# Performance work log

Measured on AMD Instinct MI355X. Metric: run time of the kernel, lower is better.

Reference implementation:

```python
import jax, jax.numpy as jnp
import numpy as np

FEATURE_DIM = 128
VALUE_DIM = 128


def setup_inputs() -> dict:
    key = jax.random.key(0)
    k1, k2, k3 = jax.random.split(key, 3)
    BH, S = 32, 4096
    q = jax.random.normal(k1, (BH, S, FEATURE_DIM), dtype=jnp.float32)
    k = jax.random.normal(k2, (BH, S, FEATURE_DIM), dtype=jnp.float32)
    v = jax.random.normal(k3, (BH, S, VALUE_DIM), dtype=jnp.float32)
    return {"q": q, "k": k, "v": v, "chunk_size": 128}


def reference(q, k, v, chunk_size):
    # q,k: [BH,S,F]; v: [BH,S,V]. Chunked fast-weight linear-attention scan:
    # out_t = q_t . (sum_{s<=t} k_s (x) v_s) / t
    BH, S, F = q.shape
    V = v.shape[-1]
    C = max(1, int(chunk_size))
    assert S % C == 0, "seq_len must be divisible by chunk_size for this reference"
    n_chunks = S // C
    # [n_chunks, BH, C, dim] for lax.scan over chunks
    qc = q.reshape(BH, n_chunks, C, F).transpose(1, 0, 2, 3)
    kc = k.reshape(BH, n_chunks, C, F).transpose(1, 0, 2, 3)
    vc = v.reshape(BH, n_chunks, C, V).transpose(1, 0, 2, 3)

    w0 = jnp.zeros((BH, F, V), dtype=q.dtype)

    def step(w_state, inputs):
        qi, ki, vi = inputs  # [BH,C,F], [BH,C,F], [BH,C,V]
        kv = jnp.einsum('bnf,bnv->bnfv', ki, vi)          # [BH,C,F,V]
        w_prefix = jnp.cumsum(kv, axis=1) + w_state[:, None]  # inclusive prefix sums
        out = jnp.einsum('bnf,bnfv->bnv', qi, w_prefix)    # [BH,C,V]
        return w_prefix[:, -1], out

    _, outs = jax.lax.scan(step, w0, (qc, kc, vc))
    out = outs.transpose(1, 0, 2, 3).reshape(BH, S, V)
    inv_counts = 1.0 / jnp.arange(1, S + 1, dtype=q.dtype)
    return out * inv_counts[None, :, None]
```

## Files before the change

### kernel.cpp

```cpp
#include <hip/hip_runtime.h>


typedef _Float16 f16;
typedef __attribute__((ext_vector_type(2))) _Float16 f16x2;
typedef __attribute__((ext_vector_type(4))) _Float16 f16x4;
typedef __attribute__((ext_vector_type(8))) _Float16 f16x8;
typedef __attribute__((ext_vector_type(16))) float f32x16;
typedef __attribute__((ext_vector_type(4))) float fv4;
typedef __attribute__((ext_vector_type(4))) int i32x4;

#define MFMA32(a, b, c) __builtin_amdgcn_mfma_f32_32x32x16_f16((a), (b), (c), 0, 0, 0)

__device__ __forceinline__ f16x4 cvt4(fv4 x) {
  f16x2 lo = __builtin_bit_cast(f16x2, __builtin_amdgcn_cvt_pkrtz(x[0], x[1]));
  f16x2 hi = __builtin_bit_cast(f16x2, __builtin_amdgcn_cvt_pkrtz(x[2], x[3]));
  return __builtin_shufflevector(lo, hi, 0, 1, 2, 3);
}

__device__ __forceinline__ int swzb(int row, int col) {
  int s = (row ^ (row >> 3)) & 7;
  return (row << 8) + ((col << 1) ^ (s << 4));
}

__device__ __forceinline__ f16x8 frag32(const f16* lds, int row, int kk, int lane) {
  int c0 = (kk << 4) + ((lane >> 5) << 3);
  return *(const f16x8*)((const char*)lds + swzb(row, c0));
}

__device__ __forceinline__ int rowf(int r, int g) {
  return (r & 3) + ((r >> 2) << 3) + (g << 2);
}

__global__ __launch_bounds__(512, 1)
void ttr_pt(const float* __restrict__ k, const float* __restrict__ v,
            f16* __restrict__ pt) {
  __shared__ f16 kT[128 * 128];
  __shared__ f16 vT[128 * 128];
  const int tid = threadIdx.x, lane = tid & 63, wave = tid >> 6;
  const int bh = blockIdx.x >> 5, c = blockIdx.x & 31;
  const float* kg = k + ((size_t)bh * 4096 + c * 128) * 128;
  const float* vg = v + ((size_t)bh * 4096 + c * 128) * 128;
  const int f0 = (tid & 31) << 2;
#pragma unroll
  for (int p = 0; p < 8; ++p) {
    int s = (p << 4) + (tid >> 5);
    fv4 xk = *(const fv4*)(kg + s * 128 + f0);
    fv4 xv = *(const fv4*)(vg + s * 128 + f0);
#pragma unroll
    for (int e = 0; e < 4; ++e) {
      *(f16*)((char*)kT + swzb(f0 + e, s)) = (f16)xk[e];
      *(f16*)((char*)vT + swzb(f0 + e, s)) = (f16)xv[e];
    }
  }
  __syncthreads();
  const int l31 = lane & 31, g = lane >> 5;
  const int mt = wave >> 1, nt0 = (wave & 1) << 1;
  f32x16 p0 = {0.f}, p1 = {0.f};
#pragma unroll
  for (int kk = 0; kk < 8; ++kk) {
    f16x8 a = frag32(vT, (mt << 5) + l31, kk, lane);
    p0 = MFMA32(a, frag32(kT, (nt0 << 5) + l31, kk, lane), p0);
    p1 = MFMA32(a, frag32(kT, ((nt0 + 1) << 5) + l31, kk, lane), p1);
  }
  f16* dst = pt + (size_t)blockIdx.x * 16384;
#pragma unroll
  for (int r = 0; r < 16; ++r) {
    int vr = (mt << 5) + rowf(r, g);
    dst[vr * 128 + (nt0 << 5) + l31] = (f16)p0[r];
    dst[vr * 128 + ((nt0 + 1) << 5) + l31] = (f16)p1[r];
  }
}

__global__ __launch_bounds__(256, 1)
void ttr_prefix(const f16* __restrict__ pt, f16* __restrict__ w) {
  __shared__ f16 xch[256 * 8];
  const int tid = threadIdx.x;
  const int bh = blockIdx.x >> 3, vs = blockIdx.x & 7;
  const int v0 = vs << 4;
  const int NT = v0 >> 5;
  const int vloc = tid >> 4, fblk = tid & 15;
  const size_t bhbase = (size_t)bh * 32 * 16384;
  const f16* src = pt + bhbase + (size_t)(v0 + vloc) * 128 + fblk * 8;
  const int kk = tid >> 5, gg = (tid >> 4) & 1, lc = tid & 15;
  f16* dstu = w + bhbase +
              (size_t)(((NT * 8 + kk) * 64) + gg * 32 + (v0 & 31) + lc) * 8;
  const int phi_w = vloc * 16 + (fblk ^ vloc);
  const int phi_r = lc * 16 + ((tid >> 4) ^ lc);
  float acc[8];
#pragma unroll
  for (int e = 0; e < 8; ++e) acc[e] = 0.f;
  for (int c = 0; c < 32; ++c) {
    f16x8 pcur = *(const f16x8*)(src + (size_t)c * 16384);
    f16x8 h;
#pragma unroll
    for (int e = 0; e < 8; ++e) h[e] = (f16)acc[e];
    *(f16x8*)(xch + phi_w * 8) = h;
    __syncthreads();
    f16x8 o = *(const f16x8*)(xch + phi_r * 8);
    *(f16x8*)(dstu + (size_t)c * 16384) = o;
    __syncthreads();
#pragma unroll
    for (int e = 0; e < 8; ++e) acc[e] += (float)pcur[e];
  }
}

__global__ __launch_bounds__(256, 3)
void ttr_out(const float* __restrict__ q, const float* __restrict__ k,
             const float* __restrict__ v, const f16* __restrict__ w,
             float* __restrict__ out) {
  __shared__ f16 k_lds[128 * 128];
  __shared__ f16 vT[64 * 128];
  const int tid = threadIdx.x, lane = tid & 63, wave = tid >> 6;
  const int l31 = lane & 31, g = lane >> 5;
  const int widx = blockIdx.x & 15;
  const int gidx = ((blockIdx.x >> 4) << 3) + (widx & 7);
  const int vh = widx >> 3;
  const int bh = gidx >> 5, c = gidx & 31;
  const float* qg = q + ((size_t)bh * 4096 + c * 128) * 128;
  const float* kg = k + ((size_t)bh * 4096 + c * 128) * 128;
  const float* vg = v + ((size_t)bh * 4096 + c * 128) * 128 + vh * 64;

  const f16* wsrc = w + (size_t)gidx * 16384 + (size_t)(vh * 2) * 4096;
  f16x8 wf0[8], wf1[8];
#pragma unroll
  for (int kk = 0; kk < 8; ++kk) {
    wf0[kk] = *(const f16x8*)(wsrc + (size_t)((kk << 6) + lane) * 8);
    wf1[kk] = *(const f16x8*)(wsrc + (size_t)(4096 + ((kk << 6) + lane) * 8));
  }

  f16x8 qf[8];
  {
    const float* qr = qg + ((wave << 5) + l31) * 128 + (g << 3);
#pragma unroll
    for (int kk = 0; kk < 8; ++kk) {
      f16x4 a = cvt4(*(const fv4*)(qr + (kk << 4)));
      f16x4 b = cvt4(*(const fv4*)(qr + (kk << 4) + 4));
      qf[kk] = __builtin_shufflevector(a, b, 0, 1, 2, 3, 4, 5, 6, 7);
    }
  }
  {
    const int c0 = (tid & 31) << 2;
#pragma unroll
    for (int p = 0; p < 16; ++p) {
      int s = (p << 3) + (tid >> 5);
      *(f16x4*)((char*)k_lds + swzb(s, c0)) = cvt4(*(const fv4*)(kg + s * 128 + c0));
    }
  }
  {
    const int c0 = (tid & 15) << 2;
#pragma unroll
    for (int p = 0; p < 8; ++p) {
      int s = (p << 4) + (tid >> 4);
      fv4 xv = *(const fv4*)(vg + s * 128 + c0);
#pragma unroll
      for (int e = 0; e < 4; ++e)
        *(f16*)((char*)vT + swzb(c0 + e, s)) = (f16)xv[e];
    }
  }
  __syncthreads();

  f32x16 o0 = {0.f}, o1 = {0.f};
#pragma unroll
  for (int kk = 0; kk < 8; ++kk) {
    o0 = MFMA32(qf[kk], wf0[kk], o0);
    o1 = MFMA32(qf[kk], wf1[kk], o1);
  }

  for (int j = 0; j <= wave; ++j) {
    f32x16 sa = {0.f};
#pragma unroll
    for (int kk = 0; kk < 8; ++kk)
      sa = MFMA32(frag32(k_lds, (j << 5) + l31, kk, lane), qf[kk], sa);
    if (j == wave) {
#pragma unroll
      for (int r = 0; r < 16; ++r)
        if (rowf(r, g) > l31) sa[r] = 0.f;
    }
    int wds[8];
#pragma unroll
    for (int t = 0; t < 8; ++t)
      wds[t] = __builtin_bit_cast(
          int, __builtin_amdgcn_cvt_pkrtz(sa[2 * t], sa[2 * t + 1]));
    int rA = __shfl_xor(g ? wds[0] : wds[2], 32, 64);
    int rB = __shfl_xor(g ? wds[1] : wds[3], 32, 64);
    int rC = __shfl_xor(g ? wds[4] : wds[6], 32, 64);
    int rD = __shfl_xor(g ? wds[5] : wds[7], 32, 64);
    i32x4 P0 = {g ? rA : wds[0], g ? rB : wds[1],
                g ? wds[2] : rA, g ? wds[3] : rB};
    i32x4 P1 = {g ? rC : wds[4], g ? rD : wds[5],
                g ? wds[6] : rC, g ? wds[7] : rD};
    f16x8 pa0 = __builtin_bit_cast(f16x8, P0);
    f16x8 pa1 = __builtin_bit_cast(f16x8, P1);
    o0 = MFMA32(pa0, frag32(vT, l31, (j << 1), lane), o0);
    o0 = MFMA32(pa1, frag32(vT, l31, (j << 1) + 1, lane), o0);
    o1 = MFMA32(pa0, frag32(vT, 32 + l31, (j << 1), lane), o1);
    o1 = MFMA32(pa1, frag32(vT, 32 + l31, (j << 1) + 1, lane), o1);
  }

  float* og = out + (((size_t)bh * 4096) + c * 128 + (wave << 5)) * 128 + vh * 64;
#pragma unroll
  for (int r = 0; r < 16; ++r) {
    int rl = rowf(r, g);
    float tg = (float)(c * 128 + (wave << 5) + rl + 1);
    float rcp = __builtin_amdgcn_rcpf(tg);
    og[rl * 128 + l31] = o0[r] * rcp;
    og[rl * 128 + 32 + l31] = o1[r] * rcp;
  }
}

extern "C" void kernel_launch(void* const* d_in, const int* in_sizes, int n_in,
                              void* d_out, int out_size, void* d_ws, size_t ws_size,
                              hipStream_t stream) {
  const float* q = (const float*)d_in[0];
  const float* k = (const float*)d_in[1];
  const float* v = (const float*)d_in[2];
  float* o = (float*)d_out;
  f16* pt = (f16*)d_ws;
  f16* w = pt + (size_t)32 * 32 * 16384;
  ttr_pt<<<dim3(1024), dim3(512), 0, stream>>>(k, v, pt);
  ttr_prefix<<<dim3(256), dim3(256), 0, stream>>>(pt, w);
  ttr_out<<<dim3(2048), dim3(256), 0, stream>>>(q, k, v, w, o);
}
```

Measured before the change: 96.07 us.

## Stage fp16 K and transposed V in workspace, load via global_load_lds

The first kernel now also writes swizzled fp16 copies of K and of the transposed V tile to workspace. The output kernel then copies those pre-laid-out tiles straight into LDS with global_load_lds, replacing the fp32 loads, conversions and scattered 2-byte transposing LDS writes. This halves the K/V bytes the output kernel reads and removes conversion work from it. In exchange the first kernel does extra stores and needs a larger workspace; a fallback path keeps the old behaviour when the workspace is too small.

New measurement: 114.6 us. 19.3% more time.

```diff
diff --git a/kernel.cpp b/kernel.cpp
--- a/kernel.cpp
+++ b/kernel.cpp
@@ -17,6 +17,12 @@
   return __builtin_shufflevector(lo, hi, 0, 1, 2, 3);
 }
 
+__device__ __forceinline__ void gll16(const void* g, void* l) {
+  __builtin_amdgcn_global_load_lds(
+      (const __attribute__((address_space(1))) void*)g,
+      (__attribute__((address_space(3))) void*)l, 16, 0, 0);
+}
+
 __device__ __forceinline__ int swzb(int row, int col) {
   int s = (row ^ (row >> 3)) & 7;
   return (row << 8) + ((col << 1) ^ (s << 4));
@@ -33,13 +39,15 @@
 
 __global__ __launch_bounds__(512, 1)
 void ttr_pt(const float* __restrict__ k, const float* __restrict__ v,
-            f16* __restrict__ pt) {
+            f16* __restrict__ pt, f16* __restrict__ k16,
+            f16* __restrict__ vt16) {
   __shared__ f16 kT[128 * 128];
   __shared__ f16 vT[128 * 128];
   const int tid = threadIdx.x, lane = tid & 63, wave = tid >> 6;
   const int bh = blockIdx.x >> 5, c = blockIdx.x & 31;
   const float* kg = k + ((size_t)bh * 4096 + c * 128) * 128;
   const float* vg = v + ((size_t)bh * 4096 + c * 128) * 128;
+  f16* kd = k16 ? k16 + (size_t)blockIdx.x * 16384 : nullptr;
   const int f0 = (tid & 31) << 2;
 #pragma unroll
   for (int p = 0; p < 8; ++p) {
@@ -51,8 +59,17 @@
       *(f16*)((char*)kT + swzb(f0 + e, s)) = (f16)xk[e];
       *(f16*)((char*)vT + swzb(f0 + e, s)) = (f16)xv[e];
     }
+    if (kd) *(f16x4*)((char*)kd + swzb(s, f0)) = cvt4(xk);
   }
   __syncthreads();
+  if (k16) {
+    f16* vd = vt16 + (size_t)blockIdx.x * 16384;
+#pragma unroll
+    for (int i = 0; i < 4; ++i) {
+      int off = (tid + (i << 9)) << 3;
+      *(f16x8*)(vd + off) = *(const f16x8*)(vT + off);
+    }
+  }
   const int l31 = lane & 31, g = lane >> 5;
   const int mt = wave >> 1, nt0 = (wave & 1) << 1;
   f32x16 p0 = {0.f}, p1 = {0.f};
@@ -104,10 +121,102 @@
   }
 }
 
+#define K3_BODY(VT_TILES)                                                     \
+  f32x16 o0 = {0.f}, o1 = {0.f};                                              \
+  _Pragma("unroll") for (int kk = 0; kk < 8; ++kk) {                          \
+    o0 = MFMA32(qf[kk], wf0[kk], o0);                                         \
+    o1 = MFMA32(qf[kk], wf1[kk], o1);                                         \
+  }                                                                           \
+  for (int j = 0; j <= wave; ++j) {                                           \
+    f32x16 sa = {0.f};                                                        \
+    _Pragma("unroll") for (int kk = 0; kk < 8; ++kk)                          \
+        sa = MFMA32(frag32(k_lds, (j << 5) + l31, kk, lane), qf[kk], sa);     \
+    if (j == wave) {                                                          \
+      _Pragma("unroll") for (int r = 0; r < 16; ++r)                          \
+          if (rowf(r, g) > l31) sa[r] = 0.f;                                  \
+    }                                                                         \
+    int wds[8];                                                               \
+    _Pragma("unroll") for (int t = 0; t < 8; ++t)                             \
+        wds[t] = __builtin_bit_cast(                                          \
+            int, __builtin_amdgcn_cvt_pkrtz(sa[2 * t], sa[2 * t + 1]));       \
+    int rA = __shfl_xor(g ? wds[0] : wds[2], 32, 64);                         \
+    int rB = __shfl_xor(g ? wds[1] : wds[3], 32, 64);                         \
+    int rC = __shfl_xor(g ? wds[4] : wds[6], 32, 64);                         \
+    int rD = __shfl_xor(g ? wds[5] : wds[7], 32, 64);                         \
+    i32x4 P0 = {g ? rA : wds[0], g ? rB : wds[1], g ? wds[2] : rA,            \
+                g ? wds[3] : rB};                                             \
+    i32x4 P1 = {g ? rC : wds[4], g ? rD : wds[5], g ? wds[6] : rC,            \
+                g ? wds[7] : rD};                                             \
+    f16x8 pa0 = __builtin_bit_cast(f16x8, P0);                                \
+    f16x8 pa1 = __builtin_bit_cast(f16x8, P1);                                \
+    o0 = MFMA32(pa0, frag32(vT, l31, (j << 1), lane), o0);                    \
+    o0 = MFMA32(pa1, frag32(vT, l31, (j << 1) + 1, lane), o0);                \
+    o1 = MFMA32(pa0, frag32(vT, 32 + l31, (j << 1), lane), o1);               \
+    o1 = MFMA32(pa1, frag32(vT, 32 + l31, (j << 1) + 1, lane), o1);           \
+  }                                                                           \
+  float* og =                                                                 \
+      out + (((size_t)bh * 4096) + c * 128 + (wave << 5)) * 128 + vh * 64;    \
+  _Pragma("unroll") for (int r = 0; r < 16; ++r) {                            \
+    int rl = rowf(r, g);                                                      \
+    float tg = (float)(c * 128 + (wave << 5) + rl + 1);                       \
+    float rcp = __builtin_amdgcn_rcpf(tg);                                    \
+    og[rl * 128 + l31] = o0[r] * rcp;                                         \
+    og[rl * 128 + 32 + l31] = o1[r] * rcp;                                    \
+  }
+
 __global__ __launch_bounds__(256, 3)
-void ttr_out(const float* __restrict__ q, const float* __restrict__ k,
-             const float* __restrict__ v, const f16* __restrict__ w,
-             float* __restrict__ out) {
+void ttr_out_gll(const float* __restrict__ q, const f16* __restrict__ k16,
+                 const f16* __restrict__ vt16, const f16* __restrict__ w,
+                 float* __restrict__ out) {
+  __shared__ f16 k_lds[128 * 128];
+  __shared__ f16 vT[64 * 128];
+  const int tid = threadIdx.x, lane = tid & 63, wave = tid >> 6;
+  const int l31 = lane & 31, g = lane >> 5;
+  const int widx = blockIdx.x & 15;
+  const int gidx = ((blockIdx.x >> 4) << 3) + (widx & 7);
+  const int vh = widx >> 3;
+  const int bh = gidx >> 5, c = gidx & 31;
+  const float* qg = q + ((size_t)bh * 4096 + c * 128) * 128;
+
+  {
+    const char* ksrc = (const char*)(k16 + (size_t)gidx * 16384);
+    const char* vsrc = (const char*)(vt16 + (size_t)gidx * 16384) + vh * 16384;
+#pragma unroll
+    for (int i = 0; i < 8; ++i) {
+      int off = (wave << 13) + (i << 10);
+      gll16(ksrc + off + lane * 16, (char*)k_lds + off);
+    }
+#pragma unroll
+    for (int i = 0; i < 4; ++i) {
+      int off = (wave << 12) + (i << 10);
+      gll16(vsrc + off + lane * 16, (char*)vT + off);
+    }
+  }
+  const f16* wsrc = w + (size_t)gidx * 16384 + (size_t)(vh * 2) * 4096;
+  f16x8 wf0[8], wf1[8];
+#pragma unroll
+  for (int kk = 0; kk < 8; ++kk) {
+    wf0[kk] = *(const f16x8*)(wsrc + (size_t)((kk << 6) + lane) * 8);
+    wf1[kk] = *(const f16x8*)(wsrc + (size_t)(4096 + ((kk << 6) + lane) * 8));
+  }
+  f16x8 qf[8];
+  {
+    const float* qr = qg + ((wave << 5) + l31) * 128 + (g << 3);
+#pragma unroll
+    for (int kk = 0; kk < 8; ++kk) {
+      f16x4 a = cvt4(*(const fv4*)(qr + (kk << 4)));
+      f16x4 b = cvt4(*(const fv4*)(qr + (kk << 4) + 4));
+      qf[kk] = __builtin_shufflevector(a, b, 0, 1, 2, 3, 4, 5, 6, 7);
+    }
+  }
+  __syncthreads();
+  K3_BODY(2)
+}
+
+__global__ __launch_bounds__(256, 3)
+void ttr_out_reg(const float* __restrict__ q, const float* __restrict__ k,
+                 const float* __restrict__ v, const f16* __restrict__ w,
+                 float* __restrict__ out) {
   __shared__ f16 k_lds[128 * 128];
   __shared__ f16 vT[64 * 128];
   const int tid = threadIdx.x, lane = tid & 63, wave = tid >> 6;
@@ -119,7 +228,6 @@
   const float* qg = q + ((size_t)bh * 4096 + c * 128) * 128;
   const float* kg = k + ((size_t)bh * 4096 + c * 128) * 128;
   const float* vg = v + ((size_t)bh * 4096 + c * 128) * 128 + vh * 64;
-
   const f16* wsrc = w + (size_t)gidx * 16384 + (size_t)(vh * 2) * 4096;
   f16x8 wf0[8], wf1[8];
 #pragma unroll
@@ -127,7 +235,6 @@
     wf0[kk] = *(const f16x8*)(wsrc + (size_t)((kk << 6) + lane) * 8);
     wf1[kk] = *(const f16x8*)(wsrc + (size_t)(4096 + ((kk << 6) + lane) * 8));
   }
-
   f16x8 qf[8];
   {
     const float* qr = qg + ((wave << 5) + l31) * 128 + (g << 3);
@@ -158,54 +265,7 @@
     }
   }
   __syncthreads();
-
-  f32x16 o0 = {0.f}, o1 = {0.f};
-#pragma unroll
-  for (int kk = 0; kk < 8; ++kk) {
-    o0 = MFMA32(qf[kk], wf0[kk], o0);
-    o1 = MFMA32(qf[kk], wf1[kk], o1);
-  }
-
-  for (int j = 0; j <= wave; ++j) {
-    f32x16 sa = {0.f};
-#pragma unroll
-    for (int kk = 0; kk < 8; ++kk)
-      sa = MFMA32(frag32(k_lds, (j << 5) + l31, kk, lane), qf[kk], sa);
-    if (j == wave) {
-#pragma unroll
-      for (int r = 0; r < 16; ++r)
-        if (rowf(r, g) > l31) sa[r] = 0.f;
-    }
-    int wds[8];
-#pragma unroll
-    for (int t = 0; t < 8; ++t)
-      wds[t] = __builtin_bit_cast(
-          int, __builtin_amdgcn_cvt_pkrtz(sa[2 * t], sa[2 * t + 1]));
-    int rA = __shfl_xor(g ? wds[0] : wds[2], 32, 64);
-    int rB = __shfl_xor(g ? wds[1] : wds[3], 32, 64);
-    int rC = __shfl_xor(g ? wds[4] : wds[6], 32, 64);
-    int rD = __shfl_xor(g ? wds[5] : wds[7], 32, 64);
-    i32x4 P0 = {g ? rA : wds[0], g ? rB : wds[1],
-                g ? wds[2] : rA, g ? wds[3] : rB};
-    i32x4 P1 = {g ? rC : wds[4], g ? rD : wds[5],
-                g ? wds[6] : rC, g ? wds[7] : rD};
-    f16x8 pa0 = __builtin_bit_cast(f16x8, P0);
-    f16x8 pa1 = __builtin_bit_cast(f16x8, P1);
-    o0 = MFMA32(pa0, frag32(vT, l31, (j << 1), lane), o0);
-    o0 = MFMA32(pa1, frag32(vT, l31, (j << 1) + 1, lane), o0);
-    o1 = MFMA32(pa0, frag32(vT, 32 + l31, (j << 1), lane), o1);
-    o1 = MFMA32(pa1, frag32(vT, 32 + l31, (j << 1) + 1, lane), o1);
-  }
-
-  float* og = out + (((size_t)bh * 4096) + c * 128 + (wave << 5)) * 128 + vh * 64;
-#pragma unroll
-  for (int r = 0; r < 16; ++r) {
-    int rl = rowf(r, g);
-    float tg = (float)(c * 128 + (wave << 5) + rl + 1);
-    float rcp = __builtin_amdgcn_rcpf(tg);
-    og[rl * 128 + l31] = o0[r] * rcp;
-    og[rl * 128 + 32 + l31] = o1[r] * rcp;
-  }
+  K3_BODY(2)
 }
 
 extern "C" void kernel_launch(void* const* d_in, const int* in_sizes, int n_in,
@@ -215,9 +275,18 @@
   const float* k = (const float*)d_in[1];
   const float* v = (const float*)d_in[2];
   float* o = (float*)d_out;
+  const size_t blk = (size_t)1024 * 16384;
   f16* pt = (f16*)d_ws;
-  f16* w = pt + (size_t)32 * 32 * 16384;
-  ttr_pt<<<dim3(1024), dim3(512), 0, stream>>>(k, v, pt);
-  ttr_prefix<<<dim3(256), dim3(256), 0, stream>>>(pt, w);
-  ttr_out<<<dim3(2048), dim3(256), 0, stream>>>(q, k, v, w, o);
-}
+  f16* w = pt + blk;
+  f16* k16 = w + blk;
+  f16* vt16 = k16 + blk;
+  if (ws_size >= 4 * blk * sizeof(f16)) {
+    ttr_pt<<<dim3(1024), dim3(512), 0, stream>>>(k, v, pt, k16, vt16);
+    ttr_prefix<<<dim3(256), dim3(256), 0, stream>>>(pt, w);
+    ttr_out_gll<<<dim3(2048), dim3(256), 0, stream>>>(q, k16, vt16, w, o);
+  } else {
+    ttr_pt<<<dim3(1024), dim3(512), 0, stream>>>(k, v, pt, nullptr, nullptr);
+    ttr_prefix<<<dim3(256), dim3(256), 0, stream>>>(pt, w);
+    ttr_out_reg<<<dim3(2048), dim3(256), 0, stream>>>(q, k, v, w, o);
+  }
+}
```
